# Kernel optimization log

Hardware: AMD Instinct MI355X
Metric: run time of the kernel (lower is better)

The kernel has to match this reference:

```python
import jax, jax.numpy as jnp
import numpy as np

NEG_SLOPE = 0.2   # PyG GATConv default negative_slope
LN_EPS = 1e-5
SOFTMAX_EPS = 1e-16  # PyG softmax denominator eps


def setup_inputs() -> dict:
    key = jax.random.key(0)
    ks = jax.random.split(key, 6)
    N, IN, OUT, H, E = 100000, 128, 64, 2, 1600000
    X = jax.random.normal(ks[0], (N, IN), dtype=jnp.float32)
    edge_index = jax.random.randint(ks[1], (2, E), 0, N, dtype=jnp.int64)
    W = jax.random.normal(ks[2], (H * OUT, IN), dtype=jnp.float32) * 0.05
    att_src = jax.random.normal(ks[3], (H, OUT), dtype=jnp.float32) * 0.05
    att_dst = jax.random.normal(ks[4], (H, OUT), dtype=jnp.float32) * 0.05
    bias = jnp.zeros((OUT,), dtype=jnp.float32)
    ln_gamma = jnp.ones((OUT,), dtype=jnp.float32)
    ln_beta = jnp.zeros((OUT,), dtype=jnp.float32)
    return {"X": X, "edge_index": edge_index, "W": W, "att_src": att_src,
            "att_dst": att_dst, "bias": bias, "ln_gamma": ln_gamma, "ln_beta": ln_beta}


def reference(X, edge_index, W, att_src, att_dst, bias, ln_gamma, ln_beta):
    N = X.shape[0]
    H, F = att_src.shape
    # PyG GATConv default: add self-loops
    loops = jnp.arange(N, dtype=edge_index.dtype)
    src = jnp.concatenate([edge_index[0], loops])  # [Et]
    dst = jnp.concatenate([edge_index[1], loops])  # [Et]
    # linear projection: x' = X @ W^T  -> [N, H, F]
    x = (X @ W.T).reshape(N, H, F)
    # per-node attention logits  [N, H]
    a_src = jnp.einsum('nhf,hf->nh', x, att_src)
    a_dst = jnp.einsum('nhf,hf->nh', x, att_dst)
    # per-edge logits, leaky relu  [Et, H]
    e = jax.nn.leaky_relu(a_src[src] + a_dst[dst], NEG_SLOPE)
    # segment softmax over incoming edges of each dst node
    m = jax.ops.segment_max(e, dst, num_segments=N)          # [N, H]
    ex = jnp.exp(e - m[dst])
    denom = jax.ops.segment_sum(ex, dst, num_segments=N)     # [N, H]
    alpha = ex / (denom[dst] + SOFTMAX_EPS)                  # [Et, H]
    # weighted scatter-add of source features
    msg = x[src] * alpha[:, :, None]                         # [Et, H, F]
    out = jax.ops.segment_sum(msg, dst, num_segments=N)      # [N, H, F]
    # concat=False -> mean over heads, then bias
    out = out.mean(axis=1) + bias                            # [N, F]
    # LayerNorm over features
    mu = out.mean(axis=-1, keepdims=True)
    var = ((out - mu) ** 2).mean(axis=-1, keepdims=True)
    h = (out - mu) * jax.lax.rsqrt(var + LN_EPS) * ln_gamma + ln_beta
    return h
```

## Files before the change

kernel.cpp:

```cpp
#include <hip/hip_runtime.h>
#include <hip/hip_bf16.h>

#define NEG_SLOPE 0.2f
#define LN_EPS 1e-5f
#define SM_EPS 1e-16f

typedef __attribute__((ext_vector_type(8))) short bf16x8;
typedef __attribute__((ext_vector_type(4))) float f32x4;

__device__ inline unsigned short f2bf(float f) {
    unsigned u = __float_as_uint(f);
    return (unsigned short)((u + 0x7FFFu + ((u >> 16) & 1u)) >> 16);
}
__device__ inline float bf_lo(unsigned int v) { return __uint_as_float(v << 16); }
__device__ inline float bf_hi(unsigned int v) { return __uint_as_float(v & 0xffff0000u); }
__device__ inline float rdlane(float v, int l) {
    return __uint_as_float(__builtin_amdgcn_readlane(__float_as_uint(v), l));
}

#define NBIN 512
#define BCAP 4864
#define SCHUNK 4096
#define CURPAD 16

__global__ __launch_bounds__(256) void k_gs(const float* __restrict__ X,
                                            const float* __restrict__ W,
                                            const float* __restrict__ att_src,
                                            const float* __restrict__ att_dst,
                                            unsigned int* __restrict__ xp,
                                            float2* __restrict__ aS,
                                            float2* __restrict__ aD,
                                            const int* __restrict__ ei,
                                            int* __restrict__ binCursor,
                                            unsigned int* __restrict__ tmp,
                                            int N, int E, int SB) {
    __shared__ __align__(16) char smem[52224];
    const int t = threadIdx.x;

    if ((int)blockIdx.x < SB) {
        int* off = (int*)smem;
        const int base = blockIdx.x * SCHUNK;

        int bn[16];
        unsigned int pe[16];
#pragma unroll
        for (int k = 0; k < 16; ++k) {
            int i = base + k * 256 + t;
            if (i < E) {
                int s = ei[i];
                int d = ei[E + i];
                bn[k] = d >> 8;
                pe[k] = ((unsigned)(d & 255) << 24) | (unsigned)s;
            } else {
                bn[k] = -1;
            }
        }

        for (int i = t; i < NBIN; i += 256) off[i] = 0;
        __syncthreads();
#pragma unroll
        for (int k = 0; k < 16; ++k)
            if (bn[k] >= 0) atomicAdd(&off[bn[k]], 1);
        __syncthreads();
        for (int i = t; i < NBIN; i += 256) {
            int h = off[i];
            off[i] = h ? (atomicAdd(&binCursor[i * CURPAD], h) + i * BCAP) : 0;
        }
        __syncthreads();
#pragma unroll
        for (int k = 0; k < 16; ++k) {
            if (bn[k] >= 0) {
                int p = atomicAdd(&off[bn[k]], 1);
                tmp[p] = pe[k];
            }
        }
        return;
    }

    unsigned short* Ws = (unsigned short*)smem;
    unsigned short* Xs = (unsigned short*)(smem + 34816);
    const int b0 = ((int)blockIdx.x - SB) * 64;
    const int lane = t & 63;
    const int w = t >> 6;
    const int c15 = lane & 15;
    const int quad = lane >> 4;

#pragma unroll
    for (int i = 0; i < 16; ++i) {
        int f = i * 256 + t;
        int nr = f >> 5;
        int q = f & 31;
        float4 v = reinterpret_cast<const float4*>(W)[nr * 32 + q];
        ushort4 b;
        b.x = f2bf(v.x); b.y = f2bf(v.y); b.z = f2bf(v.z); b.w = f2bf(v.w);
        *reinterpret_cast<ushort4*>(&Ws[nr * 136 + q * 4]) = b;
    }
#pragma unroll
    for (int i = 0; i < 8; ++i) {
        int f = i * 256 + t;
        int m = f >> 5;
        int q = f & 31;
        int gr = b0 + m;
        if (gr >= N) gr = N - 1;
        float4 v = reinterpret_cast<const float4*>(X)[(size_t)gr * 32 + q];
        ushort4 b;
        b.x = f2bf(v.x); b.y = f2bf(v.y); b.z = f2bf(v.z); b.w = f2bf(v.w);
        *reinterpret_cast<ushort4*>(&Xs[m * 136 + q * 4]) = b;
    }
    __syncthreads();

    f32x4 acc[8];
#pragma unroll
    for (int ct = 0; ct < 8; ++ct) acc[ct] = (f32x4){0.f, 0.f, 0.f, 0.f};

#pragma unroll
    for (int kc = 0; kc < 4; ++kc) {
        bf16x8 af = *reinterpret_cast<const bf16x8*>(
            &Xs[(w * 16 + c15) * 136 + kc * 32 + quad * 8]);
#pragma unroll
        for (int ct = 0; ct < 8; ++ct) {
            bf16x8 bfr = *reinterpret_cast<const bf16x8*>(
                &Ws[(ct * 16 + c15) * 136 + kc * 32 + quad * 8]);
            acc[ct] = __builtin_amdgcn_mfma_f32_16x16x32_bf16(af, bfr, acc[ct], 0, 0, 0);
        }
    }

    float attS[8], attD[8];
#pragma unroll
    for (int ct = 0; ct < 8; ++ct) {
        attS[ct] = att_src[ct * 16 + c15];
        attD[ct] = att_dst[ct * 16 + c15];
    }

#pragma unroll
    for (int r = 0; r < 4; ++r) {
        int row = b0 + w * 16 + quad * 4 + r;
        float s0 = 0.f, s1 = 0.f, d0 = 0.f, d1 = 0.f;
#pragma unroll
        for (int ct = 0; ct < 4; ++ct) {
            s0 += acc[ct][r] * attS[ct];
            d0 += acc[ct][r] * attD[ct];
            s1 += acc[ct + 4][r] * attS[ct + 4];
            d1 += acc[ct + 4][r] * attD[ct + 4];
        }
#pragma unroll
        for (int o = 1; o < 16; o <<= 1) {
            s0 += __shfl_xor(s0, o);
            s1 += __shfl_xor(s1, o);
            d0 += __shfl_xor(d0, o);
            d1 += __shfl_xor(d1, o);
        }
        if (row < N) {
#pragma unroll
            for (int ct = 0; ct < 4; ++ct) {
                unsigned int p = (unsigned int)f2bf(acc[ct][r]) |
                                 ((unsigned int)f2bf(acc[ct + 4][r]) << 16);
                xp[(size_t)row * 64 + ct * 16 + c15] = p;
            }
            if (c15 == 0) {
                aS[row] = make_float2(s0, s1);
                aD[row] = make_float2(d0, d1);
            }
        }
    }
}

__global__ __launch_bounds__(512) void k_bucket(const unsigned int* __restrict__ tmp,
                                                const int* __restrict__ binCursor,
                                                unsigned int* __restrict__ csr,
                                                unsigned int* __restrict__ rowPtr,
                                                int N) {
    __shared__ int cnt[256];
    __shared__ int cur[256];
    __shared__ int lds[4];
    const int t = threadIdx.x;
    const int b = blockIdx.x;
    const int start = b * BCAP;
    int m = binCursor[b * CURPAD];
    if (m > BCAP) m = BCAP;

    if (t < 256) cnt[t] = 0;
    __syncthreads();

    for (int k = t; k < m; k += 512) {
        atomicAdd(&cnt[tmp[start + k] >> 24], 1);
    }
    __syncthreads();

    const int lane = t & 63, w = t >> 6;
    int v = 0, incl = 0;
    if (t < 256) {
        v = cnt[t];
        incl = v;
#pragma unroll
        for (int o = 1; o < 64; o <<= 1) {
            int u = __shfl_up(incl, o);
            if (lane >= o) incl += u;
        }
        if (lane == 63) lds[w] = incl;
    }
    __syncthreads();
    if (t == 0) {
        int run = 0;
        for (int i = 0; i < 4; ++i) { int tv = lds[i]; lds[i] = run; run += tv; }
    }
    __syncthreads();
    if (t < 256) {
        int excl = lds[w] + incl - v;
        cur[t] = excl;
        int d = b * 256 + t;
        if (d < N) rowPtr[d] = (unsigned)(start + excl) | ((unsigned)v << 22);
    }
    __syncthreads();

    for (int k = t; k < m; k += 512) {
        unsigned int e = tmp[start + k];
        int p = atomicAdd(&cur[e >> 24], 1);
        csr[start + p] = e & 0x00FFFFFFu;
    }
}

__global__ __launch_bounds__(256) void k_agg(const unsigned int* __restrict__ xp,
                                             const float2* __restrict__ aS,
                                             const float2* __restrict__ aD,
                                             const unsigned int* __restrict__ rowPtr,
                                             const unsigned int* __restrict__ csr,
                                             const float* __restrict__ bias,
                                             const float* __restrict__ gamma,
                                             const float* __restrict__ beta,
                                             float* __restrict__ out, int N) {
    const int w = threadIdx.x >> 6, lane = threadIdx.x & 63;
    const int n = blockIdx.x * 4 + w;
    if (n >= N) return;

    const float* aSf = (const float*)aS;

    float2 a = aS[n];
    float2 ad2 = aD[n];
    float f0 = a.x + ad2.x; f0 = fmaxf(f0, NEG_SLOPE * f0);
    float f1 = a.y + ad2.y; f1 = fmaxf(f1, NEG_SLOPE * f1);
    float us0 = __expf(f0), us1 = __expf(f1);

    unsigned int vself = xp[((unsigned)n << 6) | lane];
    float S0 = us0 * bf_lo(vself);
    float S1 = us1 * bf_hi(vself);
    float D0 = us0, D1 = us1;

    unsigned int pr = rowPtr[n];
    const int jb = (int)(pr & 0x3FFFFFu);
    const int deg = (int)(pr >> 22);
    const int je = jb + deg;
    const int nb = (deg + 7) >> 3;

    const int eq = lane & 7;
    const int hsel = (lane >> 3) & 1;
    const float adv = hsel ? ad2.y : ad2.x;

    float Dacc = 0.f;
    int j = jb;
    unsigned int cc[8];
    unsigned int myc = 0;

    if (nb > 0) {
        int ju = __builtin_amdgcn_readfirstlane(jb);
        int last = __builtin_amdgcn_readfirstlane(je - 1);
#pragma unroll
        for (int q = 0; q < 8; ++q) {
            int idx = ju + q; if (idx > last) idx = last;
            cc[q] = csr[idx];
        }
        int mi = ju + eq; if (mi > last) mi = last;
        myc = csr[mi];
    }

    for (int bI = 0; bI < nb; ++bI) {
        const int limit = je - j;
        float av = aSf[(myc << 1) | (unsigned)hsel];
        unsigned int v[8];
#pragma unroll
        for (int q = 0; q < 8; ++q)
            v[q] = (xp + ((size_t)cc[q] << 6))[lane];
        unsigned int cn[8], mn;
        {
            int jn = (bI + 1 < nb) ? (j + 8) : jb;
            int ju = __builtin_amdgcn_readfirstlane(jn);
            int last = __builtin_amdgcn_readfirstlane(je - 1);
#pragma unroll
            for (int q = 0; q < 8; ++q) {
                int idx = ju + q; if (idx > last) idx = last;
                cn[q] = csr[idx];
            }
            int mi = ju + eq; if (mi > last) mi = last;
            mn = csr[mi];
        }
        float g = av + adv; g = fmaxf(g, NEG_SLOPE * g);
        float u = (eq < limit) ? __expf(g) : 0.f;
        Dacc += u;
#pragma unroll
        for (int q = 0; q < 8; ++q) {
            float u0 = rdlane(u, q);
            float u1 = rdlane(u, q + 8);
            S0 = fmaf(u0, bf_lo(v[q]), S0);
            S1 = fmaf(u1, bf_hi(v[q]), S1);
        }
#pragma unroll
        for (int q = 0; q < 8; ++q) cc[q] = cn[q];
        myc = mn;
        j += 8;
    }

    Dacc += __shfl_xor(Dacc, 1);
    Dacc += __shfl_xor(Dacc, 2);
    Dacc += __shfl_xor(Dacc, 4);
    D0 += rdlane(Dacc, 0);
    D1 += rdlane(Dacc, 8);

    float o = (0.5f / (D0 + SM_EPS)) * S0 + (0.5f / (D1 + SM_EPS)) * S1 + bias[lane];

    float mu = o;
#pragma unroll
    for (int d = 32; d > 0; d >>= 1) mu += __shfl_xor(mu, d);
    mu *= (1.0f / 64.0f);
    float dv = o - mu;
    float var = dv * dv;
#pragma unroll
    for (int d = 32; d > 0; d >>= 1) var += __shfl_xor(var, d);
    var *= (1.0f / 64.0f);
    out[(size_t)n * 64 + lane] = dv * rsqrtf(var + LN_EPS) * gamma[lane] + beta[lane];
}

extern "C" void kernel_launch(void* const* d_in, const int* in_sizes, int n_in,
                              void* d_out, int out_size, void* d_ws, size_t ws_size,
                              hipStream_t stream) {
    const float* X        = (const float*)d_in[0];
    const int*   ei       = (const int*)d_in[1];
    const float* W        = (const float*)d_in[2];
    const float* att_src  = (const float*)d_in[3];
    const float* att_dst  = (const float*)d_in[4];
    const float* bias     = (const float*)d_in[5];
    const float* ln_gamma = (const float*)d_in[6];
    const float* ln_beta  = (const float*)d_in[7];
    float* out = (float*)d_out;

    const int N = in_sizes[0] / 128;
    const int E = in_sizes[1] / 2;
    const int NBUCK = (N + 255) / 256;
    const int SB = (E + SCHUNK - 1) / SCHUNK;
    const int GB = (N + 63) / 64;

    char* ws = (char*)d_ws;
    size_t off = 0;
    auto alloc = [&](size_t bytes) {
        size_t o = off;
        off += (bytes + 255) & ~(size_t)255;
        return o;
    };
    unsigned int* xp     = (unsigned int*)(ws + alloc((size_t)N * 64 * 4));
    float2* aS           = (float2*)(ws + alloc((size_t)N * 8));
    float2* aD           = (float2*)(ws + alloc((size_t)N * 8));
    unsigned int* rowPtr = (unsigned int*)(ws + alloc((size_t)N * 4));
    unsigned int* csr    = (unsigned int*)(ws + alloc((size_t)NBIN * BCAP * 4));
    unsigned int* tmp    = (unsigned int*)(ws + alloc((size_t)NBIN * BCAP * 4));
    int* binCursor       = (int*)(ws + alloc(NBIN * CURPAD * 4));

    hipMemsetAsync(binCursor, 0, (size_t)NBIN * CURPAD * 4, stream);
    k_gs<<<SB + GB, 256, 0, stream>>>(X, W, att_src, att_dst, xp, aS, aD,
                                      ei, binCursor, tmp, N, E, SB);
    k_bucket<<<NBUCK, 512, 0, stream>>>(tmp, binCursor, csr, rowPtr, N);
    k_agg<<<(N + 3) / 4, 256, 0, stream>>>(xp, aS, aD, rowPtr, csr,
                                           bias, ln_gamma, ln_beta, out, N);
}
```

Measured before the change: 215.0 us.

## Precompute per-node exponentials so edge weights need only multiplies in aggregation

The producer kernel now stores exp(a) and exp(slope*a) for both heads of each node's source and destination logits. The aggregation kernel then forms each edge weight as a product of two such factors, choosing the branch by comparing the product with 1, which removes the per-edge exp. Both head weights are packed into one bf16x2 lane value so a single readlane serves both heads, and the software-prefetched source factors are now one float4 load. The risks are extra storage and load traffic for the float4 arrays, bf16 rounding of the softmax weights, and possible overflow because the exponentials are no longer shifted by the segment max.

```diff
diff --git a/kernel.cpp b/kernel.cpp
--- a/kernel.cpp
+++ b/kernel.cpp
@@ -14,9 +14,6 @@
 }
 __device__ inline float bf_lo(unsigned int v) { return __uint_as_float(v << 16); }
 __device__ inline float bf_hi(unsigned int v) { return __uint_as_float(v & 0xffff0000u); }
-__device__ inline float rdlane(float v, int l) {
-    return __uint_as_float(__builtin_amdgcn_readlane(__float_as_uint(v), l));
-}
 
 #define NBIN 512
 #define BCAP 4864
@@ -28,8 +25,8 @@
                                             const float* __restrict__ att_src,
                                             const float* __restrict__ att_dst,
                                             unsigned int* __restrict__ xp,
-                                            float2* __restrict__ aS,
-                                            float2* __restrict__ aD,
+                                            float4* __restrict__ PS,
+                                            float4* __restrict__ PD,
                                             const int* __restrict__ ei,
                                             int* __restrict__ binCursor,
                                             unsigned int* __restrict__ tmp,
@@ -158,8 +155,10 @@
                 xp[(size_t)row * 64 + ct * 16 + c15] = p;
             }
             if (c15 == 0) {
-                aS[row] = make_float2(s0, s1);
-                aD[row] = make_float2(d0, d1);
+                PS[row] = make_float4(__expf(s0), __expf(NEG_SLOPE * s0),
+                                      __expf(s1), __expf(NEG_SLOPE * s1));
+                PD[row] = make_float4(__expf(d0), __expf(NEG_SLOPE * d0),
+                                      __expf(d1), __expf(NEG_SLOPE * d1));
             }
         }
     }
@@ -221,8 +220,8 @@
 }
 
 __global__ __launch_bounds__(256) void k_agg(const unsigned int* __restrict__ xp,
-                                             const float2* __restrict__ aS,
-                                             const float2* __restrict__ aD,
+                                             const float4* __restrict__ PS,
+                                             const float4* __restrict__ PD,
                                              const unsigned int* __restrict__ rowPtr,
                                              const unsigned int* __restrict__ csr,
                                              const float* __restrict__ bias,
@@ -233,13 +232,13 @@
     const int n = blockIdx.x * 4 + w;
     if (n >= N) return;
 
-    const float* aSf = (const float*)aS;
-
-    float2 a = aS[n];
-    float2 ad2 = aD[n];
-    float f0 = a.x + ad2.x; f0 = fmaxf(f0, NEG_SLOPE * f0);
-    float f1 = a.y + ad2.y; f1 = fmaxf(f1, NEG_SLOPE * f1);
-    float us0 = __expf(f0), us1 = __expf(f1);
+    float4 pd = PD[n];
+    float4 pss = PS[n];
+
+    float sm0 = pss.x * pd.x, smp0 = pss.y * pd.y;
+    float sm1 = pss.z * pd.z, smp1 = pss.w * pd.w;
+    float us0 = (sm0 >= 1.f) ? sm0 : smp0;
+    float us1 = (sm1 >= 1.f) ? sm1 : smp1;
 
     unsigned int vself = xp[((unsigned)n << 6) | lane];
     float S0 = us0 * bf_lo(vself);
@@ -253,13 +252,12 @@
     const int nb = (deg + 7) >> 3;
 
     const int eq = lane & 7;
-    const int hsel = (lane >> 3) & 1;
-    const float adv = hsel ? ad2.y : ad2.x;
-
-    float Dacc = 0.f;
+
+    float Dacc0 = 0.f, Dacc1 = 0.f;
     int j = jb;
     unsigned int cc[8];
     unsigned int myc = 0;
+    float4 psv = make_float4(0.f, 0.f, 0.f, 0.f);
 
     if (nb > 0) {
         int ju = __builtin_amdgcn_readfirstlane(jb);
@@ -271,11 +269,11 @@
         }
         int mi = ju + eq; if (mi > last) mi = last;
         myc = csr[mi];
+        psv = PS[myc];
     }
 
     for (int bI = 0; bI < nb; ++bI) {
         const int limit = je - j;
-        float av = aSf[(myc << 1) | (unsigned)hsel];
         unsigned int v[8];
 #pragma unroll
         for (int q = 0; q < 8; ++q)
@@ -293,27 +291,41 @@
             int mi = ju + eq; if (mi > last) mi = last;
             mn = csr[mi];
         }
-        float g = av + adv; g = fmaxf(g, NEG_SLOPE * g);
-        float u = (eq < limit) ? __expf(g) : 0.f;
-        Dacc += u;
+        float4 psn = PS[mn];
+
+        float m0 = psv.x * pd.x, mp0 = psv.y * pd.y;
+        float m1 = psv.z * pd.z, mp1 = psv.w * pd.w;
+        float u0 = (m0 >= 1.f) ? m0 : mp0;
+        float u1 = (m1 >= 1.f) ? m1 : mp1;
+        unsigned int u01;
+        asm("v_cvt_pk_bf16_f32 %0, %1, %2" : "=v"(u01) : "v"(u0), "v"(u1));
+        u01 = (eq < limit) ? u01 : 0u;
+        Dacc0 += bf_lo(u01);
+        Dacc1 += bf_hi(u01);
+
 #pragma unroll
         for (int q = 0; q < 8; ++q) {
-            float u0 = rdlane(u, q);
-            float u1 = rdlane(u, q + 8);
-            S0 = fmaf(u0, bf_lo(v[q]), S0);
-            S1 = fmaf(u1, bf_hi(v[q]), S1);
+            unsigned int ub = (unsigned)__builtin_amdgcn_readlane((int)u01, q);
+            float w0 = __uint_as_float(ub << 16);
+            float w1 = __uint_as_float(ub & 0xffff0000u);
+            S0 = fmaf(w0, bf_lo(v[q]), S0);
+            S1 = fmaf(w1, bf_hi(v[q]), S1);
         }
 #pragma unroll
         for (int q = 0; q < 8; ++q) cc[q] = cn[q];
         myc = mn;
+        psv = psn;
         j += 8;
     }
 
-    Dacc += __shfl_xor(Dacc, 1);
-    Dacc += __shfl_xor(Dacc, 2);
-    Dacc += __shfl_xor(Dacc, 4);
-    D0 += rdlane(Dacc, 0);
-    D1 += rdlane(Dacc, 8);
+    Dacc0 += __shfl_xor(Dacc0, 1);
+    Dacc0 += __shfl_xor(Dacc0, 2);
+    Dacc0 += __shfl_xor(Dacc0, 4);
+    Dacc1 += __shfl_xor(Dacc1, 1);
+    Dacc1 += __shfl_xor(Dacc1, 2);
+    Dacc1 += __shfl_xor(Dacc1, 4);
+    D0 += Dacc0;
+    D1 += Dacc1;
 
     float o = (0.5f / (D0 + SM_EPS)) * S0 + (0.5f / (D1 + SM_EPS)) * S1 + bias[lane];
 
@@ -356,17 +368,17 @@
         return o;
     };
     unsigned int* xp     = (unsigned int*)(ws + alloc((size_t)N * 64 * 4));
-    float2* aS           = (float2*)(ws + alloc((size_t)N * 8));
-    float2* aD           = (float2*)(ws + alloc((size_t)N * 8));
+    float4* PS           = (float4*)(ws + alloc((size_t)N * 16));
+    float4* PD           = (float4*)(ws + alloc((size_t)N * 16));
     unsigned int* rowPtr = (unsigned int*)(ws + alloc((size_t)N * 4));
     unsigned int* csr    = (unsigned int*)(ws + alloc((size_t)NBIN * BCAP * 4));
     unsigned int* tmp    = (unsigned int*)(ws + alloc((size_t)NBIN * BCAP * 4));
     int* binCursor       = (int*)(ws + alloc(NBIN * CURPAD * 4));
 
     hipMemsetAsync(binCursor, 0, (size_t)NBIN * CURPAD * 4, stream);
-    k_gs<<<SB + GB, 256, 0, stream>>>(X, W, att_src, att_dst, xp, aS, aD,
+    k_gs<<<SB + GB, 256, 0, stream>>>(X, W, att_src, att_dst, xp, PS, PD,
                                       ei, binCursor, tmp, N, E, SB);
     k_bucket<<<NBUCK, 512, 0, stream>>>(tmp, binCursor, csr, rowPtr, N);
-    k_agg<<<(N + 3) / 4, 256, 0, stream>>>(xp, aS, aD, rowPtr, csr,
+    k_agg<<<(N + 3) / 4, 256, 0, stream>>>(xp, PS, PD, rowPtr, csr,
                                            bias, ln_gamma, ln_beta, out, N);
 }
```

New measurement: 219.2 us. About the same (+2.0%).
